# Kernel tuning notes

Measured on AMD Instinct MI355X. Metric: run time of the kernel, lower is better.

## Reference

```python
import jax, jax.numpy as jnp
import numpy as np

DIM = 256
HEADS = 4


def setup_inputs() -> dict:
    key = jax.random.key(0)
    k1, k2, k3, k4, k5 = jax.random.split(key, 5)
    x = jax.random.normal(k1, (8, DIM, 128, 128), dtype=jnp.float32)
    s_in = 1.0 / np.sqrt(DIM)
    Wqkv = jax.random.normal(k2, (DIM, 3 * DIM), dtype=jnp.float32) * s_in
    bqkv = jax.random.normal(k3, (3 * DIM,), dtype=jnp.float32) * 0.02
    Wproj = jax.random.normal(k4, (DIM, DIM), dtype=jnp.float32) * s_in
    bproj = jax.random.normal(k5, (DIM,), dtype=jnp.float32) * 0.02
    return {"x": x, "Wqkv": Wqkv, "bqkv": bqkv, "Wproj": Wproj, "bproj": bproj}


def reference(x, Wqkv, bqkv, Wproj, bproj):
    b, c, h, w = x.shape
    hd = c // HEADS  # head dim
    scale = hd ** -0.5
    # axis='h': (b c h w) -> (b*w, h, c)
    x_r = jnp.transpose(x, (0, 3, 2, 1)).reshape(b * w, h, c)
    qkv = x_r @ Wqkv + bqkv                              # [B, S, 3c]
    qkv = qkv.reshape(b * w, h, 3, HEADS, hd)
    qkv = jnp.transpose(qkv, (2, 0, 3, 1, 4))            # [3, B, H, S, d]
    q, k, v = qkv[0], qkv[1], qkv[2]
    attn = jax.nn.softmax(jnp.einsum('bhqd,bhkd->bhqk', q, k) * scale, axis=-1)
    out = jnp.einsum('bhqk,bhkd->bhqd', attn, v)         # [B, H, S, d]
    out = jnp.transpose(out, (0, 2, 1, 3)).reshape(b * w, h, c)
    out = out @ Wproj + bproj
    # (b*w, h, c) -> (b, c, h, w)
    out = out.reshape(b, w, h, c)
    return jnp.transpose(out, (0, 3, 2, 1))
```

## Files before the change

### kernel.cpp

```cpp
#include <hip/hip_runtime.h>


typedef _Float16 h4 __attribute__((ext_vector_type(4)));
typedef _Float16 h8 __attribute__((ext_vector_type(8)));
typedef float f4 __attribute__((ext_vector_type(4)));
typedef unsigned int u4 __attribute__((ext_vector_type(4)));

#define MFMA32(a, b, c) __builtin_amdgcn_mfma_f32_16x16x32_f16((a), (b), (c), 0, 0, 0)

__device__ __forceinline__ void gll16(const _Float16* g, _Float16* l) {
  __builtin_amdgcn_global_load_lds(
      (const __attribute__((address_space(1))) void*)g,
      (__attribute__((address_space(3))) void*)l, 16, 0, 0);
}

__global__ __launch_bounds__(256) void prep_w(const float* __restrict__ Wqkv,
                                              const float* __restrict__ Wproj,
                                              _Float16* __restrict__ wqt,
                                              _Float16* __restrict__ wpt) {
  int i = blockIdx.x * 256 + threadIdx.x;
  if (i < 768 * 256) {
    int f = i >> 8, c = i & 255;
    wqt[i] = (_Float16)Wqkv[c * 768 + f];
  } else {
    int j = i - 768 * 256;
    int f = j >> 8, c = j & 255;
    wpt[j] = (_Float16)Wproj[c * 256 + f];
  }
}

__global__ __launch_bounds__(256) void prep_x(const float* __restrict__ x,
                                              _Float16* __restrict__ xt,
                                              int b_base) {
  const int h = blockIdx.x, bl = blockIdx.y;
  const int b = b_base + bl;
  const int tid = threadIdx.x;
  __shared__ __align__(16) _Float16 sT[256 * 132];

  const int wj = tid & 31, cg = tid >> 5;
#pragma unroll
  for (int ci = 0; ci < 32; ++ci) {
    const int c = cg * 32 + ci;
    f4 v = *(const f4*)(x + (((long)b * 256 + c) * 128 + h) * 128 + wj * 4);
    h4 o;
    o[0] = (_Float16)v[0]; o[1] = (_Float16)v[1];
    o[2] = (_Float16)v[2]; o[3] = (_Float16)v[3];
    *(h4*)(sT + c * 132 + wj * 4) = o;
  }
  __syncthreads();

#pragma unroll
  for (int tt2 = tid; tt2 < 512; tt2 += 256) {
    const int cb = tt2 & 31, wb = tt2 >> 5;
    h8 r[8];
#pragma unroll
    for (int j = 0; j < 8; ++j)
      r[j] = *(const h8*)(sT + (cb * 8 + j) * 132 + wb * 8);
#pragma unroll
    for (int i = 0; i < 8; ++i) {
      h8 o;
#pragma unroll
      for (int j = 0; j < 8; ++j) o[j] = r[j][i];
      const int w = wb * 8 + i;
      *(h8*)(xt + ((long)bl * 16384 + w * 128 + h) * 256 + cb * 8) = o;
    }
  }
}

__global__ __launch_bounds__(256, 4) void k1_qkv(const _Float16* __restrict__ xt,
                                                 const _Float16* __restrict__ wqt,
                                                 const float* __restrict__ bqkv,
                                                 _Float16* __restrict__ qkv,
                                                 int nb) {
  const int wg = blockIdx.x;
  const int xcd = wg & 7, gseq = wg >> 3;
  const int ft = gseq % 6, ghi = gseq / 6;
  const int G = ghi * 8 + xcd;
  const int tt = G & 127, bl = G >> 7;

  const int tid = threadIdx.x;
  const int lane = tid & 63, wv = tid >> 6;
  const int g = lane >> 4, l16 = lane & 15;
  const int wr = wv >> 1, wc = wv & 1;
  const int f0 = ft * 128;

  __shared__ __align__(16) char smem[34816];
  _Float16* sA = (_Float16*)smem;
  _Float16* sB = sA + 128 * 64;
  _Float16* sO = sA;

  f4 acc[4][4];
#pragma unroll
  for (int mt = 0; mt < 4; ++mt)
#pragma unroll
    for (int nt = 0; nt < 4; ++nt)
#pragma unroll
      for (int r = 0; r < 4; ++r) acc[mt][nt][r] = 0.f;

  const _Float16* Ab = wqt + (long)f0 * 256;
  const _Float16* Bb = xt + ((long)bl * 16384 + tt * 128) * 256;
  const int r0 = wv * 32;
  const int rl = lane >> 3, ch = (lane & 7) * 8;

  for (int kc = 0; kc < 4; ++kc) {
    const int c0 = kc * 64;
#pragma unroll
    for (int i = 0; i < 4; ++i) {
      const int row = r0 + i * 8 + rl;
      gll16(Ab + (long)row * 256 + c0 + ch, sA + (r0 + i * 8) * 64);
      gll16(Bb + (long)row * 256 + c0 + ch, sB + (r0 + i * 8) * 64);
    }
    __syncthreads();
#pragma unroll
    for (int ks = 0; ks < 2; ++ks) {
      const int k = ks * 32 + 8 * g;
      h8 af[4], bf[4];
#pragma unroll
      for (int mt = 0; mt < 4; ++mt)
        af[mt] = *(const h8*)(sA + (wr * 64 + mt * 16 + l16) * 64 + k);
#pragma unroll
      for (int nt = 0; nt < 4; ++nt)
        bf[nt] = *(const h8*)(sB + (wc * 64 + nt * 16 + l16) * 64 + k);
#pragma unroll
      for (int mt = 0; mt < 4; ++mt)
#pragma unroll
        for (int nt = 0; nt < 4; ++nt)
          acc[mt][nt] = MFMA32(af[mt], bf[nt], acc[mt][nt]);
    }
    __syncthreads();
  }

#pragma unroll
  for (int mt = 0; mt < 4; ++mt) {
    f4 bb = *(const f4*)(bqkv + f0 + wr * 64 + mt * 16 + 4 * g);
#pragma unroll
    for (int nt = 0; nt < 4; ++nt) {
      const int tl = wc * 64 + nt * 16 + l16;
#pragma unroll
      for (int r = 0; r < 4; ++r)
        sO[tl * 136 + wr * 64 + mt * 16 + 4 * g + r] =
            (_Float16)(acc[mt][nt][r] + bb[r]);
    }
  }
  __syncthreads();

  const int hh = tid >> 1, dh = (tid & 1) * 32;
#pragma unroll
  for (int h2 = 0; h2 < 2; ++h2) {
    const int fh = f0 + h2 * 64;
    const int qi = fh >> 8, head = (fh >> 6) & 3;
    _Float16* dst =
        qkv + (((long)(qi * nb + bl) * 4 + head) * 128 + tt) * 8192 + hh * 64 + dh;
    const _Float16* s = sO + hh * 136 + h2 * 64 + dh;
#pragma unroll
    for (int e = 0; e < 4; ++e)
      *(u4*)(dst + e * 8) = *(const u4*)(s + e * 8);
  }
}

__global__ __launch_bounds__(256) void k2_attn(const _Float16* __restrict__ qkv,
                                               _Float16* __restrict__ attnout,
                                               int nb) {
  const int w = blockIdx.x, head = blockIdx.y, bl = blockIdx.z;
  const int tid = threadIdx.x;
  const int lane = tid & 63, wv = tid >> 6;
  const int g = lane >> 4, l16 = lane & 15;

  __shared__ __align__(16) char smem[(128 * 72 * 2 + 64 * 136) * 2];
  _Float16* sQ = (_Float16*)smem;
  _Float16* sK = sQ + 128 * 72;
  _Float16* sVT = sK + 128 * 72;
  _Float16* sP = sQ;
  _Float16* sO = sQ;

  const long base = (((long)bl * 4 + head) * 128 + w) * 8192;
  const long QS = (long)nb * 4 * 128 * 8192;
  const _Float16* qg = qkv + base;
  const _Float16* kg = qkv + base + QS;
  const _Float16* vg = qkv + base + 2 * QS;

#pragma unroll
  for (int i = 0; i < 4; ++i) {
    int u = tid + 256 * i;
    int hh = u >> 3, dq = u & 7;
    *(u4*)(sQ + hh * 72 + dq * 8) = *(const u4*)(qg + hh * 64 + dq * 8);
    *(u4*)(sK + hh * 72 + dq * 8) = *(const u4*)(kg + hh * 64 + dq * 8);
  }
  {
    const int hh = tid & 127, dc = tid >> 7;
#pragma unroll
    for (int jj = 0; jj < 4; ++jj) {
      u4 vv = *(const u4*)(vg + hh * 64 + dc * 32 + jj * 8);
      const _Float16* pe = (const _Float16*)&vv;
#pragma unroll
      for (int e = 0; e < 8; ++e)
        sVT[(dc * 32 + jj * 8 + e) * 136 + hh] = pe[e];
    }
  }
  __syncthreads();

  f4 accS[8][2];
  for (int i = 0; i < 8; ++i)
    for (int jt = 0; jt < 2; ++jt)
      for (int r = 0; r < 4; ++r) accS[i][jt][r] = 0.f;
#pragma unroll
  for (int ks = 0; ks < 2; ++ks) {
    const int k = ks * 32 + 8 * g;
    h8 af[8], bf[2];
#pragma unroll
    for (int i = 0; i < 8; ++i)
      af[i] = *(const h8*)(sK + (i * 16 + l16) * 72 + k);
#pragma unroll
    for (int jt = 0; jt < 2; ++jt)
      bf[jt] = *(const h8*)(sQ + (wv * 32 + jt * 16 + l16) * 72 + k);
#pragma unroll
    for (int i = 0; i < 8; ++i)
#pragma unroll
      for (int jt = 0; jt < 2; ++jt)
        accS[i][jt] = MFMA32(af[i], bf[jt], accS[i][jt]);
  }

  float rinv[2];
#pragma unroll
  for (int jt = 0; jt < 2; ++jt) {
    float m = -1e30f;
    for (int i = 0; i < 8; ++i)
      for (int r = 0; r < 4; ++r) m = fmaxf(m, accS[i][jt][r]);
    m = fmaxf(m, __shfl_xor(m, 16));
    m = fmaxf(m, __shfl_xor(m, 32));
    float s = 0.f;
    for (int i = 0; i < 8; ++i)
      for (int r = 0; r < 4; ++r) {
        float p = __expf((accS[i][jt][r] - m) * 0.125f);
        accS[i][jt][r] = p;
        s += p;
      }
    s += __shfl_xor(s, 16);
    s += __shfl_xor(s, 32);
    rinv[jt] = 1.0f / s;
  }

  __syncthreads();
#pragma unroll
  for (int jt = 0; jt < 2; ++jt) {
    const int hq = wv * 32 + jt * 16 + l16;
#pragma unroll
    for (int i = 0; i < 8; ++i) {
      h4 pv;
      pv[0] = (_Float16)accS[i][jt][0];
      pv[1] = (_Float16)accS[i][jt][1];
      pv[2] = (_Float16)accS[i][jt][2];
      pv[3] = (_Float16)accS[i][jt][3];
      *(h4*)(sP + hq * 136 + i * 16 + 4 * g) = pv;
    }
  }
  __syncthreads();

  f4 accO[4][2];
  for (int mt = 0; mt < 4; ++mt)
    for (int jt = 0; jt < 2; ++jt)
      for (int r = 0; r < 4; ++r) accO[mt][jt][r] = 0.f;
#pragma unroll
  for (int i2 = 0; i2 < 4; ++i2) {
    const int k = i2 * 32 + 8 * g;
    h8 av[4], pb[2];
#pragma unroll
    for (int mt = 0; mt < 4; ++mt)
      av[mt] = *(const h8*)(sVT + (mt * 16 + l16) * 136 + k);
#pragma unroll
    for (int jt = 0; jt < 2; ++jt)
      pb[jt] = *(const h8*)(sP + (wv * 32 + jt * 16 + l16) * 136 + k);
#pragma unroll
    for (int mt = 0; mt < 4; ++mt)
#pragma unroll
      for (int jt = 0; jt < 2; ++jt)
        accO[mt][jt] = MFMA32(av[mt], pb[jt], accO[mt][jt]);
  }

  __syncthreads();
#pragma unroll
  for (int mt = 0; mt < 4; ++mt)
#pragma unroll
    for (int jt = 0; jt < 2; ++jt)
#pragma unroll
      for (int r = 0; r < 4; ++r)
        sO[(wv * 32 + jt * 16 + l16) * 72 + mt * 16 + 4 * g + r] =
            (_Float16)(accO[mt][jt][r] * rinv[jt]);
  __syncthreads();

  const int hh = tid >> 1, d0 = (tid & 1) * 32;
  const _Float16* s = sO + hh * 72 + d0;
  _Float16* dst = attnout + ((long)bl * 16384 + hh * 128 + w) * 256 + head * 64 + d0;
#pragma unroll
  for (int e = 0; e < 4; ++e)
    *(u4*)(dst + e * 8) = *(const u4*)(s + e * 8);
}

__global__ __launch_bounds__(256, 4) void k3_proj(const _Float16* __restrict__ attnout,
                                                  const _Float16* __restrict__ wpt,
                                                  const float* __restrict__ bproj,
                                                  float* __restrict__ out,
                                                  int b_base, int nb) {
  const int ct = blockIdx.x, tt = blockIdx.y, bl = blockIdx.z;
  const int b = b_base + bl;
  const int tid = threadIdx.x;
  const int lane = tid & 63, wv = tid >> 6;
  const int g = lane >> 4, l16 = lane & 15;
  const int wr = wv >> 1, wc = wv & 1;
  const int co0 = ct * 128;
  const long t0 = (long)tt * 128;

  __shared__ __align__(16) char smem[33792];
  _Float16* sA = (_Float16*)smem;
  _Float16* sB = sA + 128 * 64;
  float* sOut = (float*)smem;

  f4 acc[4][4];
#pragma unroll
  for (int mt = 0; mt < 4; ++mt)
#pragma unroll
    for (int nt = 0; nt < 4; ++nt)
#pragma unroll
      for (int r = 0; r < 4; ++r) acc[mt][nt][r] = 0.f;

  const _Float16* Ab = wpt + (long)co0 * 256;
  const _Float16* Bb = attnout + ((long)bl * 16384 + t0) * 256;
  const int r0 = wv * 32;
  const int rl = lane >> 3, ch = (lane & 7) * 8;

  for (int kc = 0; kc < 4; ++kc) {
    const int c0 = kc * 64;
#pragma unroll
    for (int i = 0; i < 4; ++i) {
      const int row = r0 + i * 8 + rl;
      gll16(Ab + (long)row * 256 + c0 + ch, sA + (r0 + i * 8) * 64);
      gll16(Bb + (long)row * 256 + c0 + ch, sB + (r0 + i * 8) * 64);
    }
    __syncthreads();
#pragma unroll
    for (int ks = 0; ks < 2; ++ks) {
      const int k = ks * 32 + 8 * g;
      h8 af[4], bf[4];
#pragma unroll
      for (int mt = 0; mt < 4; ++mt)
        af[mt] = *(const h8*)(sA + (wr * 64 + mt * 16 + l16) * 64 + k);
#pragma unroll
      for (int nt = 0; nt < 4; ++nt)
        bf[nt] = *(const h8*)(sB + (wc * 64 + nt * 16 + l16) * 64 + k);
#pragma unroll
      for (int mt = 0; mt < 4; ++mt)
#pragma unroll
        for (int nt = 0; nt < 4; ++nt)
          acc[mt][nt] = MFMA32(af[mt], bf[nt], acc[mt][nt]);
    }
    __syncthreads();
  }

#pragma unroll
  for (int h2 = 0; h2 < 2; ++h2) {
    if (h2) __syncthreads();
    if (wr == h2) {
#pragma unroll
      for (int mt = 0; mt < 4; ++mt) {
        f4 bb = *(const f4*)(bproj + co0 + h2 * 64 + mt * 16 + 4 * g);
#pragma unroll
        for (int nt = 0; nt < 4; ++nt)
#pragma unroll
          for (int r = 0; r < 4; ++r)
            sOut[(mt * 16 + 4 * g + r) * 132 + wc * 64 + nt * 16 + l16] =
                acc[mt][nt][r] + bb[r];
      }
    }
    __syncthreads();
    const int row = tid >> 2, seg = (tid & 3) * 32;
    const float* s = sOut + row * 132 + seg;
    float* dst = out + ((long)b * 256 + co0 + h2 * 64 + row) * 16384 + t0 + seg;
#pragma unroll
    for (int e = 0; e < 8; ++e)
      *(f4*)(dst + e * 4) = *(const f4*)(s + e * 4);
  }
}

extern "C" void kernel_launch(void* const* d_in, const int* in_sizes, int n_in,
                              void* d_out, int out_size, void* d_ws, size_t ws_size,
                              hipStream_t stream) {
  const float* x = (const float*)d_in[0];
  const float* Wqkv = (const float*)d_in[1];
  const float* bqkv = (const float*)d_in[2];
  const float* Wproj = (const float*)d_in[3];
  const float* bproj = (const float*)d_in[4];
  float* out = (float*)d_out;

  char* ws = (char*)d_ws;
  const long WQT = 393216L, WPT = 131072L;
  const long PER_B = 25165824L + 8388608L;
  long nb_l = ((long)ws_size - (WQT + WPT)) / PER_B;
  int nb = nb_l < 1 ? 1 : (nb_l > 8 ? 8 : (int)nb_l);

  _Float16* wqt = (_Float16*)ws;
  _Float16* wpt = (_Float16*)(ws + WQT);
  _Float16* qkv = (_Float16*)(ws + WQT + WPT);
  _Float16* shared = (_Float16*)(ws + WQT + WPT + (long)nb * 25165824L);
  _Float16* xt = shared;
  _Float16* attnout = shared;

  prep_w<<<1024, 256, 0, stream>>>(Wqkv, Wproj, wqt, wpt);

  for (int b0 = 0; b0 < 8; b0 += nb) {
    int nbv = (8 - b0 < nb) ? (8 - b0) : nb;
    prep_x<<<dim3(128, nbv), 256, 0, stream>>>(x, xt, b0);
    k1_qkv<<<768 * nbv, 256, 0, stream>>>(xt, wqt, bqkv, qkv, nbv);
    k2_attn<<<dim3(128, 4, nbv), 256, 0, stream>>>(qkv, attnout, nbv);
    k3_proj<<<dim3(2, 128, nbv), 256, 0, stream>>>(attnout, wpt, bproj, out, b0, nbv);
  }
}
```

Baseline: 254.9 us.

## Fuse x transpose/convert into QKV GEMM and keep X tile in registers

Removes the separate prep_x kernel and the xt fp16 intermediate buffer. Each k1f block now reads an fp32 x slice (one h row, 64 w positions, all channels) straight from global memory, transposes and converts it in LDS, then holds the B-operand fragments in registers while looping over all six 128-wide output feature tiles. This saves a full write and re-read of the transposed activations and one launch, and reuses the X tile across every Wqkv tile. In exchange it uses more LDS and registers per block (occupancy hint lowered to 2), performs a strided LDS transpose, and has fewer blocks, each doing more serial work.

```diff
diff --git a/kernel.cpp b/kernel.cpp
--- a/kernel.cpp
+++ b/kernel.cpp
@@ -29,132 +29,120 @@
   }
 }
 
-__global__ __launch_bounds__(256) void prep_x(const float* __restrict__ x,
-                                              _Float16* __restrict__ xt,
-                                              int b_base) {
-  const int h = blockIdx.x, bl = blockIdx.y;
+__global__ __launch_bounds__(256, 2) void k1f(const float* __restrict__ x,
+                                              const _Float16* __restrict__ wqt,
+                                              const float* __restrict__ bqkv,
+                                              _Float16* __restrict__ qkv,
+                                              int b_base, int nb) {
+  const int wg = blockIdx.x;
+  const int xcd = wg & 7, seq = wg >> 3;
+  const int id = xcd * (nb * 32) + seq;
+  const int hb = id & 127;
+  const int rest = id >> 7;
+  const int wh = rest & 1, bl = rest >> 1;
   const int b = b_base + bl;
-  const int tid = threadIdx.x;
-  __shared__ __align__(16) _Float16 sT[256 * 132];
-
-  const int wj = tid & 31, cg = tid >> 5;
-#pragma unroll
-  for (int ci = 0; ci < 32; ++ci) {
-    const int c = cg * 32 + ci;
-    f4 v = *(const f4*)(x + (((long)b * 256 + c) * 128 + h) * 128 + wj * 4);
-    h4 o;
-    o[0] = (_Float16)v[0]; o[1] = (_Float16)v[1];
-    o[2] = (_Float16)v[2]; o[3] = (_Float16)v[3];
-    *(h4*)(sT + c * 132 + wj * 4) = o;
-  }
-  __syncthreads();
-
-#pragma unroll
-  for (int tt2 = tid; tt2 < 512; tt2 += 256) {
-    const int cb = tt2 & 31, wb = tt2 >> 5;
-    h8 r[8];
-#pragma unroll
-    for (int j = 0; j < 8; ++j)
-      r[j] = *(const h8*)(sT + (cb * 8 + j) * 132 + wb * 8);
-#pragma unroll
-    for (int i = 0; i < 8; ++i) {
-      h8 o;
-#pragma unroll
-      for (int j = 0; j < 8; ++j) o[j] = r[j][i];
-      const int w = wb * 8 + i;
-      *(h8*)(xt + ((long)bl * 16384 + w * 128 + h) * 256 + cb * 8) = o;
-    }
-  }
-}
-
-__global__ __launch_bounds__(256, 4) void k1_qkv(const _Float16* __restrict__ xt,
-                                                 const _Float16* __restrict__ wqt,
-                                                 const float* __restrict__ bqkv,
-                                                 _Float16* __restrict__ qkv,
-                                                 int nb) {
-  const int wg = blockIdx.x;
-  const int xcd = wg & 7, gseq = wg >> 3;
-  const int ft = gseq % 6, ghi = gseq / 6;
-  const int G = ghi * 8 + xcd;
-  const int tt = G & 127, bl = G >> 7;
+  const int w0 = wh * 64;
 
   const int tid = threadIdx.x;
   const int lane = tid & 63, wv = tid >> 6;
   const int g = lane >> 4, l16 = lane & 15;
   const int wr = wv >> 1, wc = wv & 1;
-  const int f0 = ft * 128;
-
-  __shared__ __align__(16) char smem[34816];
+
+  __shared__ __align__(16) char smem[67584];
   _Float16* sA = (_Float16*)smem;
-  _Float16* sB = sA + 128 * 64;
-  _Float16* sO = sA;
-
-  f4 acc[4][4];
-#pragma unroll
-  for (int mt = 0; mt < 4; ++mt)
-#pragma unroll
-    for (int nt = 0; nt < 4; ++nt)
-#pragma unroll
-      for (int r = 0; r < 4; ++r) acc[mt][nt][r] = 0.f;
-
-  const _Float16* Ab = wqt + (long)f0 * 256;
-  const _Float16* Bb = xt + ((long)bl * 16384 + tt * 128) * 256;
+  _Float16* sXT = sA + 128 * 64;
+  _Float16* sO = sXT + 64 * 264;
+
+  {
+    const int r4 = tid >> 2, j0 = tid & 3;
+#pragma unroll
+    for (int p = 0; p < 4; ++p) {
+      const int c = p * 64 + r4;
+      const float* src = x + (((long)b * 256 + c) * 128 + hb) * 128 + w0;
+      f4 v[4];
+#pragma unroll
+      for (int k = 0; k < 4; ++k) v[k] = *(const f4*)(src + (j0 + 4 * k) * 4);
+#pragma unroll
+      for (int k = 0; k < 4; ++k)
+#pragma unroll
+        for (int i = 0; i < 4; ++i)
+          sXT[((j0 + 4 * k) * 4 + i) * 264 + c] = (_Float16)v[k][i];
+    }
+  }
+  __syncthreads();
+
+  h8 bfr[4][2][2];
+#pragma unroll
+  for (int kc = 0; kc < 4; ++kc)
+#pragma unroll
+    for (int ks = 0; ks < 2; ++ks)
+#pragma unroll
+      for (int nt = 0; nt < 2; ++nt) {
+        const int t = wc * 32 + nt * 16 + l16;
+        bfr[kc][ks][nt] =
+            *(const h8*)(sXT + t * 264 + kc * 64 + ks * 32 + 8 * g);
+      }
+
   const int r0 = wv * 32;
   const int rl = lane >> 3, ch = (lane & 7) * 8;
-
-  for (int kc = 0; kc < 4; ++kc) {
-    const int c0 = kc * 64;
-#pragma unroll
-    for (int i = 0; i < 4; ++i) {
-      const int row = r0 + i * 8 + rl;
-      gll16(Ab + (long)row * 256 + c0 + ch, sA + (r0 + i * 8) * 64);
-      gll16(Bb + (long)row * 256 + c0 + ch, sB + (r0 + i * 8) * 64);
+  const int wl = tid >> 2, dc = tid & 3;
+
+  for (int ft = 0; ft < 6; ++ft) {
+    const int f0 = ft * 128;
+    f4 acc[4][2];
+#pragma unroll
+    for (int mt = 0; mt < 4; ++mt)
+#pragma unroll
+      for (int nt = 0; nt < 2; ++nt)
+#pragma unroll
+        for (int r = 0; r < 4; ++r) acc[mt][nt][r] = 0.f;
+
+    for (int kc = 0; kc < 4; ++kc) {
+#pragma unroll
+      for (int i = 0; i < 4; ++i) {
+        const int row = r0 + i * 8 + rl;
+        gll16(wqt + (long)(f0 + row) * 256 + kc * 64 + ch, sA + (r0 + i * 8) * 64);
+      }
+      __syncthreads();
+#pragma unroll
+      for (int ks = 0; ks < 2; ++ks) {
+        h8 af[4];
+#pragma unroll
+        for (int mt = 0; mt < 4; ++mt)
+          af[mt] = *(const h8*)(sA + (wr * 64 + mt * 16 + l16) * 64 + ks * 32 + 8 * g);
+#pragma unroll
+        for (int mt = 0; mt < 4; ++mt)
+#pragma unroll
+          for (int nt = 0; nt < 2; ++nt)
+            acc[mt][nt] = MFMA32(af[mt], bfr[kc][ks][nt], acc[mt][nt]);
+      }
+      __syncthreads();
+    }
+
+#pragma unroll
+    for (int mt = 0; mt < 4; ++mt) {
+      f4 bb = *(const f4*)(bqkv + f0 + wr * 64 + mt * 16 + 4 * g);
+#pragma unroll
+      for (int nt = 0; nt < 2; ++nt) {
+        const int tl = wc * 32 + nt * 16 + l16;
+#pragma unroll
+        for (int r = 0; r < 4; ++r)
+          sO[tl * 136 + wr * 64 + mt * 16 + 4 * g + r] =
+              (_Float16)(acc[mt][nt][r] + bb[r]);
+      }
     }
     __syncthreads();
 #pragma unroll
-    for (int ks = 0; ks < 2; ++ks) {
-      const int k = ks * 32 + 8 * g;
-      h8 af[4], bf[4];
-#pragma unroll
-      for (int mt = 0; mt < 4; ++mt)
-        af[mt] = *(const h8*)(sA + (wr * 64 + mt * 16 + l16) * 64 + k);
-#pragma unroll
-      for (int nt = 0; nt < 4; ++nt)
-        bf[nt] = *(const h8*)(sB + (wc * 64 + nt * 16 + l16) * 64 + k);
-#pragma unroll
-      for (int mt = 0; mt < 4; ++mt)
-#pragma unroll
-        for (int nt = 0; nt < 4; ++nt)
-          acc[mt][nt] = MFMA32(af[mt], bf[nt], acc[mt][nt]);
+    for (int h2 = 0; h2 < 2; ++h2) {
+      const int fh = f0 + h2 * 64;
+      const int qi = fh >> 8, head = (fh >> 6) & 3;
+      _Float16* dst = qkv + (((long)(qi * nb + bl) * 4 + head) * 128 + w0 + wl) * 8192 +
+                      hb * 64 + dc * 16;
+      const _Float16* s = sO + wl * 136 + h2 * 64 + dc * 16;
+      *(u4*)dst = *(const u4*)s;
+      *(u4*)(dst + 8) = *(const u4*)(s + 8);
     }
     __syncthreads();
-  }
-
-#pragma unroll
-  for (int mt = 0; mt < 4; ++mt) {
-    f4 bb = *(const f4*)(bqkv + f0 + wr * 64 + mt * 16 + 4 * g);
-#pragma unroll
-    for (int nt = 0; nt < 4; ++nt) {
-      const int tl = wc * 64 + nt * 16 + l16;
-#pragma unroll
-      for (int r = 0; r < 4; ++r)
-        sO[tl * 136 + wr * 64 + mt * 16 + 4 * g + r] =
-            (_Float16)(acc[mt][nt][r] + bb[r]);
-    }
-  }
-  __syncthreads();
-
-  const int hh = tid >> 1, dh = (tid & 1) * 32;
-#pragma unroll
-  for (int h2 = 0; h2 < 2; ++h2) {
-    const int fh = f0 + h2 * 64;
-    const int qi = fh >> 8, head = (fh >> 6) & 3;
-    _Float16* dst =
-        qkv + (((long)(qi * nb + bl) * 4 + head) * 128 + tt) * 8192 + hh * 64 + dh;
-    const _Float16* s = sO + hh * 136 + h2 * 64 + dh;
-#pragma unroll
-    for (int e = 0; e < 4; ++e)
-      *(u4*)(dst + e * 8) = *(const u4*)(s + e * 8);
   }
 }
 
@@ -187,14 +175,14 @@
     *(u4*)(sK + hh * 72 + dq * 8) = *(const u4*)(kg + hh * 64 + dq * 8);
   }
   {
-    const int hh = tid & 127, dc = tid >> 7;
+    const int hh = tid & 127, dcv = tid >> 7;
 #pragma unroll
     for (int jj = 0; jj < 4; ++jj) {
-      u4 vv = *(const u4*)(vg + hh * 64 + dc * 32 + jj * 8);
+      u4 vv = *(const u4*)(vg + hh * 64 + dcv * 32 + jj * 8);
       const _Float16* pe = (const _Float16*)&vv;
 #pragma unroll
       for (int e = 0; e < 8; ++e)
-        sVT[(dc * 32 + jj * 8 + e) * 136 + hh] = pe[e];
+        sVT[(dcv * 32 + jj * 8 + e) * 136 + hh] = pe[e];
     }
   }
   __syncthreads();
@@ -400,16 +388,13 @@
   _Float16* wqt = (_Float16*)ws;
   _Float16* wpt = (_Float16*)(ws + WQT);
   _Float16* qkv = (_Float16*)(ws + WQT + WPT);
-  _Float16* shared = (_Float16*)(ws + WQT + WPT + (long)nb * 25165824L);
-  _Float16* xt = shared;
-  _Float16* attnout = shared;
+  _Float16* attnout = (_Float16*)(ws + WQT + WPT + (long)nb * 25165824L);
 
   prep_w<<<1024, 256, 0, stream>>>(Wqkv, Wproj, wqt, wpt);
 
   for (int b0 = 0; b0 < 8; b0 += nb) {
     int nbv = (8 - b0 < nb) ? (8 - b0) : nb;
-    prep_x<<<dim3(128, nbv), 256, 0, stream>>>(x, xt, b0);
-    k1_qkv<<<768 * nbv, 256, 0, stream>>>(xt, wqt, bqkv, qkv, nbv);
+    k1f<<<nbv * 256, 256, 0, stream>>>(x, wqt, bqkv, qkv, b0, nbv);
     k2_attn<<<dim3(128, 4, nbv), 256, 0, stream>>>(qkv, attnout, nbv);
     k3_proj<<<dim3(2, 128, nbv), 256, 0, stream>>>(attnout, wpt, bproj, out, b0, nbv);
   }
```

Result: slower. 267.6 us (+5.0%).

## Fuse QKV projection into attention kernel and swizzle LDS tiles

Applied to the files above, without the earlier changes.

Merges the QKV GEMM and the attention kernel into one kernel. Each workgroup computes Q, K and V for one (batch, w, head) tile directly into shared memory and then runs attention on it, so the fp16 qkv intermediate is no longer written to and read back from global memory. It also XOR-swizzles the LDS layout of the GEMM tiles in both the fused kernel and the projection kernel to reduce bank conflicts. In exchange, the x tile is reloaded once per head (4x redundant x reads), LDS grows to about 54KB per workgroup, and the 12x2 accumulator array raises register pressure and may lower occupancy.

```diff
diff --git a/kernel.cpp b/kernel.cpp
--- a/kernel.cpp
+++ b/kernel.cpp
@@ -67,134 +67,92 @@
   }
 }
 
-__global__ __launch_bounds__(256, 4) void k1_qkv(const _Float16* __restrict__ xt,
-                                                 const _Float16* __restrict__ wqt,
-                                                 const float* __restrict__ bqkv,
-                                                 _Float16* __restrict__ qkv,
-                                                 int nb) {
+__global__ __launch_bounds__(256) void k12(const _Float16* __restrict__ xt,
+                                           const _Float16* __restrict__ wqt,
+                                           const float* __restrict__ bqkv,
+                                           _Float16* __restrict__ attnout,
+                                           int nb) {
   const int wg = blockIdx.x;
-  const int xcd = wg & 7, gseq = wg >> 3;
-  const int ft = gseq % 6, ghi = gseq / 6;
-  const int G = ghi * 8 + xcd;
-  const int tt = G & 127, bl = G >> 7;
+  const int xcd = wg & 7, seq = wg >> 3;
+  const int id = xcd * (nb * 64) + seq;
+  const int head = id & 3;
+  const int w = (id >> 2) & 127;
+  const int bl = id >> 9;
 
   const int tid = threadIdx.x;
   const int lane = tid & 63, wv = tid >> 6;
   const int g = lane >> 4, l16 = lane & 15;
-  const int wr = wv >> 1, wc = wv & 1;
-  const int f0 = ft * 128;
-
-  __shared__ __align__(16) char smem[34816];
+
+  __shared__ __align__(16) char smem[54272];
   _Float16* sA = (_Float16*)smem;
-  _Float16* sB = sA + 128 * 64;
-  _Float16* sO = sA;
-
-  f4 acc[4][4];
-#pragma unroll
-  for (int mt = 0; mt < 4; ++mt)
-#pragma unroll
-    for (int nt = 0; nt < 4; ++nt)
+  _Float16* sB = (_Float16*)(smem + 24576);
+  _Float16* sQ = (_Float16*)smem;
+  _Float16* sK = (_Float16*)(smem + 18432);
+  _Float16* sVT = (_Float16*)(smem + 36864);
+  _Float16* sP = sQ;
+  _Float16* sO = sQ;
+
+  const int rl = lane >> 3;
+  const int chs = ((lane & 7) ^ rl) * 8;
+  const int kx = (l16 & 7) * 8;
+
+  f4 acc[12][2];
+#pragma unroll
+  for (int mt = 0; mt < 12; ++mt)
+#pragma unroll
+    for (int nt = 0; nt < 2; ++nt)
 #pragma unroll
       for (int r = 0; r < 4; ++r) acc[mt][nt][r] = 0.f;
 
-  const _Float16* Ab = wqt + (long)f0 * 256;
-  const _Float16* Bb = xt + ((long)bl * 16384 + tt * 128) * 256;
-  const int r0 = wv * 32;
-  const int rl = lane >> 3, ch = (lane & 7) * 8;
+  const _Float16* Bx = xt + ((long)bl * 16384 + w * 128) * 256;
 
   for (int kc = 0; kc < 4; ++kc) {
     const int c0 = kc * 64;
 #pragma unroll
+    for (int i = 0; i < 6; ++i) {
+      const int row = wv * 48 + i * 8 + rl;
+      const int fglob = (row >> 6) * 256 + head * 64 + (row & 63);
+      gll16(wqt + (long)fglob * 256 + c0 + chs, sA + (wv * 48 + i * 8) * 64);
+    }
+#pragma unroll
     for (int i = 0; i < 4; ++i) {
-      const int row = r0 + i * 8 + rl;
-      gll16(Ab + (long)row * 256 + c0 + ch, sA + (r0 + i * 8) * 64);
-      gll16(Bb + (long)row * 256 + c0 + ch, sB + (r0 + i * 8) * 64);
+      const int trow = wv * 32 + i * 8 + rl;
+      gll16(Bx + (long)trow * 256 + c0 + chs, sB + (wv * 32 + i * 8) * 64);
     }
     __syncthreads();
 #pragma unroll
     for (int ks = 0; ks < 2; ++ks) {
-      const int k = ks * 32 + 8 * g;
-      h8 af[4], bf[4];
-#pragma unroll
-      for (int mt = 0; mt < 4; ++mt)
-        af[mt] = *(const h8*)(sA + (wr * 64 + mt * 16 + l16) * 64 + k);
-#pragma unroll
-      for (int nt = 0; nt < 4; ++nt)
-        bf[nt] = *(const h8*)(sB + (wc * 64 + nt * 16 + l16) * 64 + k);
-#pragma unroll
-      for (int mt = 0; mt < 4; ++mt)
-#pragma unroll
-        for (int nt = 0; nt < 4; ++nt)
-          acc[mt][nt] = MFMA32(af[mt], bf[nt], acc[mt][nt]);
-    }
-    __syncthreads();
-  }
-
-#pragma unroll
-  for (int mt = 0; mt < 4; ++mt) {
-    f4 bb = *(const f4*)(bqkv + f0 + wr * 64 + mt * 16 + 4 * g);
-#pragma unroll
-    for (int nt = 0; nt < 4; ++nt) {
-      const int tl = wc * 64 + nt * 16 + l16;
-#pragma unroll
-      for (int r = 0; r < 4; ++r)
-        sO[tl * 136 + wr * 64 + mt * 16 + 4 * g + r] =
-            (_Float16)(acc[mt][nt][r] + bb[r]);
-    }
-  }
-  __syncthreads();
-
-  const int hh = tid >> 1, dh = (tid & 1) * 32;
-#pragma unroll
-  for (int h2 = 0; h2 < 2; ++h2) {
-    const int fh = f0 + h2 * 64;
-    const int qi = fh >> 8, head = (fh >> 6) & 3;
-    _Float16* dst =
-        qkv + (((long)(qi * nb + bl) * 4 + head) * 128 + tt) * 8192 + hh * 64 + dh;
-    const _Float16* s = sO + hh * 136 + h2 * 64 + dh;
-#pragma unroll
-    for (int e = 0; e < 4; ++e)
-      *(u4*)(dst + e * 8) = *(const u4*)(s + e * 8);
-  }
-}
-
-__global__ __launch_bounds__(256) void k2_attn(const _Float16* __restrict__ qkv,
-                                               _Float16* __restrict__ attnout,
-                                               int nb) {
-  const int w = blockIdx.x, head = blockIdx.y, bl = blockIdx.z;
-  const int tid = threadIdx.x;
-  const int lane = tid & 63, wv = tid >> 6;
-  const int g = lane >> 4, l16 = lane & 15;
-
-  __shared__ __align__(16) char smem[(128 * 72 * 2 + 64 * 136) * 2];
-  _Float16* sQ = (_Float16*)smem;
-  _Float16* sK = sQ + 128 * 72;
-  _Float16* sVT = sK + 128 * 72;
-  _Float16* sP = sQ;
-  _Float16* sO = sQ;
-
-  const long base = (((long)bl * 4 + head) * 128 + w) * 8192;
-  const long QS = (long)nb * 4 * 128 * 8192;
-  const _Float16* qg = qkv + base;
-  const _Float16* kg = qkv + base + QS;
-  const _Float16* vg = qkv + base + 2 * QS;
-
-#pragma unroll
-  for (int i = 0; i < 4; ++i) {
-    int u = tid + 256 * i;
-    int hh = u >> 3, dq = u & 7;
-    *(u4*)(sQ + hh * 72 + dq * 8) = *(const u4*)(qg + hh * 64 + dq * 8);
-    *(u4*)(sK + hh * 72 + dq * 8) = *(const u4*)(kg + hh * 64 + dq * 8);
-  }
-  {
-    const int hh = tid & 127, dc = tid >> 7;
-#pragma unroll
-    for (int jj = 0; jj < 4; ++jj) {
-      u4 vv = *(const u4*)(vg + hh * 64 + dc * 32 + jj * 8);
-      const _Float16* pe = (const _Float16*)&vv;
-#pragma unroll
-      for (int e = 0; e < 8; ++e)
-        sVT[(dc * 32 + jj * 8 + e) * 136 + hh] = pe[e];
+      const int kk = (ks * 32 + 8 * g) ^ kx;
+      h8 bf[2];
+#pragma unroll
+      for (int nt = 0; nt < 2; ++nt)
+        bf[nt] = *(const h8*)(sB + (wv * 32 + nt * 16 + l16) * 64 + kk);
+#pragma unroll
+      for (int mt = 0; mt < 12; ++mt) {
+        h8 af = *(const h8*)(sA + (mt * 16 + l16) * 64 + kk);
+#pragma unroll
+        for (int nt = 0; nt < 2; ++nt)
+          acc[mt][nt] = MFMA32(af, bf[nt], acc[mt][nt]);
+      }
+    }
+    __syncthreads();
+  }
+
+#pragma unroll
+  for (int mt = 0; mt < 12; ++mt) {
+    const int qi = mt >> 2;
+    f4 bb = *(const f4*)(bqkv + qi * 256 + head * 64 + (mt & 3) * 16 + 4 * g);
+#pragma unroll
+    for (int nt = 0; nt < 2; ++nt) {
+      const int t = wv * 32 + nt * 16 + l16;
+#pragma unroll
+      for (int r = 0; r < 4; ++r) {
+        const int d = (mt & 3) * 16 + 4 * g + r;
+        const _Float16 val = (_Float16)(acc[mt][nt][r] + bb[r]);
+        if (qi == 0) sQ[t * 72 + d] = val;
+        else if (qi == 1) sK[t * 72 + d] = val;
+        else sVT[d * 136 + t] = val;
+      }
     }
   }
   __syncthreads();
@@ -326,27 +284,29 @@
   const _Float16* Ab = wpt + (long)co0 * 256;
   const _Float16* Bb = attnout + ((long)bl * 16384 + t0) * 256;
   const int r0 = wv * 32;
-  const int rl = lane >> 3, ch = (lane & 7) * 8;
+  const int rl = lane >> 3;
+  const int chs = ((lane & 7) ^ rl) * 8;
+  const int kx = (l16 & 7) * 8;
 
   for (int kc = 0; kc < 4; ++kc) {
     const int c0 = kc * 64;
 #pragma unroll
     for (int i = 0; i < 4; ++i) {
       const int row = r0 + i * 8 + rl;
-      gll16(Ab + (long)row * 256 + c0 + ch, sA + (r0 + i * 8) * 64);
-      gll16(Bb + (long)row * 256 + c0 + ch, sB + (r0 + i * 8) * 64);
+      gll16(Ab + (long)row * 256 + c0 + chs, sA + (r0 + i * 8) * 64);
+      gll16(Bb + (long)row * 256 + c0 + chs, sB + (r0 + i * 8) * 64);
     }
     __syncthreads();
 #pragma unroll
     for (int ks = 0; ks < 2; ++ks) {
-      const int k = ks * 32 + 8 * g;
+      const int kk = (ks * 32 + 8 * g) ^ kx;
       h8 af[4], bf[4];
 #pragma unroll
       for (int mt = 0; mt < 4; ++mt)
-        af[mt] = *(const h8*)(sA + (wr * 64 + mt * 16 + l16) * 64 + k);
+        af[mt] = *(const h8*)(sA + (wr * 64 + mt * 16 + l16) * 64 + kk);
 #pragma unroll
       for (int nt = 0; nt < 4; ++nt)
-        bf[nt] = *(const h8*)(sB + (wc * 64 + nt * 16 + l16) * 64 + k);
+        bf[nt] = *(const h8*)(sB + (wc * 64 + nt * 16 + l16) * 64 + kk);
 #pragma unroll
       for (int mt = 0; mt < 4; ++mt)
 #pragma unroll
@@ -393,24 +353,21 @@
 
   char* ws = (char*)d_ws;
   const long WQT = 393216L, WPT = 131072L;
-  const long PER_B = 25165824L + 8388608L;
+  const long PER_B = 8388608L + 8388608L;
   long nb_l = ((long)ws_size - (WQT + WPT)) / PER_B;
   int nb = nb_l < 1 ? 1 : (nb_l > 8 ? 8 : (int)nb_l);
 
   _Float16* wqt = (_Float16*)ws;
   _Float16* wpt = (_Float16*)(ws + WQT);
-  _Float16* qkv = (_Float16*)(ws + WQT + WPT);
-  _Float16* shared = (_Float16*)(ws + WQT + WPT + (long)nb * 25165824L);
-  _Float16* xt = shared;
-  _Float16* attnout = shared;
+  _Float16* xt = (_Float16*)(ws + WQT + WPT);
+  _Float16* attnout = (_Float16*)(ws + WQT + WPT + (long)nb * 8388608L);
 
   prep_w<<<1024, 256, 0, stream>>>(Wqkv, Wproj, wqt, wpt);
 
   for (int b0 = 0; b0 < 8; b0 += nb) {
     int nbv = (8 - b0 < nb) ? (8 - b0) : nb;
     prep_x<<<dim3(128, nbv), 256, 0, stream>>>(x, xt, b0);
-    k1_qkv<<<768 * nbv, 256, 0, stream>>>(xt, wqt, bqkv, qkv, nbv);
-    k2_attn<<<dim3(128, 4, nbv), 256, 0, stream>>>(qkv, attnout, nbv);
+    k12<<<nbv * 512, 256, 0, stream>>>(xt, wqt, bqkv, attnout, nbv);
     k3_proj<<<dim3(2, 128, nbv), 256, 0, stream>>>(attnout, wpt, bproj, out, b0, nbv);
   }
 }
```

New measurement: 221.1 us. -13.3%, faster.
